# Performance work log

Measured on AMD Instinct MI355X. Metric: run time of the kernel, lower is better.

Reference implementation:

```python
import jax, jax.numpy as jnp
import numpy as np
import math

B, S, D, H, DH = 1, 2048, 2048, 16, 64  # batch, seq, d_model, n_heads, d_head
LAMBDA_INIT = 0.8
EPS = 1e-5


def setup_inputs() -> dict:
    key = jax.random.key(0)
    ks = jax.random.split(key, 10)
    w_scale = 0.02
    inner = 2 * DH * H  # == D here
    return {
        "x": jax.random.normal(ks[0], (B, S, D), dtype=jnp.float32),
        "Wq": jax.random.normal(ks[1], (D, inner), dtype=jnp.float32) * w_scale,
        "Wk": jax.random.normal(ks[2], (D, inner), dtype=jnp.float32) * w_scale,
        "Wv": jax.random.normal(ks[3], (D, inner), dtype=jnp.float32) * w_scale,
        "Wo": jax.random.normal(ks[4], (inner, D), dtype=jnp.float32) * w_scale,
        "lambda_q1": jax.random.normal(ks[5], (DH,), dtype=jnp.float32) * 0.1,
        "lambda_k1": jax.random.normal(ks[6], (DH,), dtype=jnp.float32) * 0.1,
        "lambda_q2": jax.random.normal(ks[7], (DH,), dtype=jnp.float32) * 0.1,
        "lambda_k2": jax.random.normal(ks[8], (DH,), dtype=jnp.float32) * 0.1,
        "gn_weight": jnp.ones((inner,), dtype=jnp.float32),
        "gn_bias": jnp.zeros((inner,), dtype=jnp.float32),
    }


def reference(x, Wq, Wk, Wv, Wo, lambda_q1, lambda_k1, lambda_q2, lambda_k2,
              gn_weight, gn_bias):
    b, s, _ = x.shape
    dh = lambda_q1.shape[0]
    h = Wq.shape[1] // (2 * dh)
    scale = 1.0 / math.sqrt(dh)

    q = (x @ Wq).reshape(b, s, h, 2, dh)
    k = (x @ Wk).reshape(b, s, h, 2, dh)
    v = (x @ Wv).reshape(b, s, h, 2 * dh)

    # [B,H,S,dh]
    q1 = jnp.swapaxes(q[..., 0, :], 1, 2)
    q2 = jnp.swapaxes(q[..., 1, :], 1, 2)
    k1 = jnp.swapaxes(k[..., 0, :], 1, 2)
    k2 = jnp.swapaxes(k[..., 1, :], 1, 2)
    vh = jnp.swapaxes(v, 1, 2)  # [B,H,S,2*dh]

    score1 = jnp.einsum("bhsd,bhtd->bhst", q1, k1) * scale
    score2 = jnp.einsum("bhsd,bhtd->bhst", q2, k2) * scale
    attn1 = jax.nn.softmax(score1, axis=-1)
    attn2 = jax.nn.softmax(score2, axis=-1)

    lam = (jnp.exp(jnp.sum(lambda_q1 * lambda_k1))
           - jnp.exp(jnp.sum(lambda_q2 * lambda_k2)) + LAMBDA_INIT)

    out = jnp.einsum("bhst,bhtd->bhsd", attn1 - lam * attn2, vh)  # [B,H,S,2dh]
    out = jnp.swapaxes(out, 1, 2)  # [B,S,H,2dh]

    # GroupNorm: n_heads groups over the channel dim, per token
    mu = jnp.mean(out, axis=-1, keepdims=True)
    var = jnp.var(out, axis=-1, keepdims=True)
    out = (out - mu) * jax.lax.rsqrt(var + EPS)
    gw = gn_weight.reshape(h, 2 * dh)
    gb = gn_bias.reshape(h, 2 * dh)
    out = out * gw + gb

    out = out * (1.0 - LAMBDA_INIT)
    return out.reshape(b, s, -1) @ Wo
```

## Files before the change

### kernel.cpp

```cpp
#include <hip/hip_runtime.h>
#include <hip/hip_bf16.h>

typedef unsigned short u16;
typedef __attribute__((ext_vector_type(8))) short short8;
typedef __attribute__((ext_vector_type(4))) short short4v;
typedef __attribute__((ext_vector_type(4))) float f32x4;

#define S_DIM 2048
#define D_DIM 2048
#define H_NUM 16
#define DH_NUM 64

#if __has_builtin(__builtin_amdgcn_exp2f)
#define EXP2(x) __builtin_amdgcn_exp2f(x)
#else
#define EXP2(x) exp2f(x)
#endif

__device__ __forceinline__ u16 f2bf(float f) {
    union { float f; unsigned u; } x; x.f = f;
    unsigned r = x.u + 0x7fff + ((x.u >> 16) & 1);
    return (u16)(r >> 16);
}

__device__ __forceinline__ unsigned pk_bf16(float a, float b) {
    union { __hip_bfloat162 h; unsigned u; } cv;
    float2 t; t.x = a; t.y = b;
    cv.h = __float22bfloat162_rn(t);
    return cv.u;
}

__device__ __forceinline__ void lane_swap32(unsigned &a, unsigned &b) {
    asm("v_permlane32_swap_b32 %0, %1" : "+v"(a), "+v"(b));
}
__device__ __forceinline__ void lane_swap16(unsigned &a, unsigned &b) {
    asm("v_permlane16_swap_b32 %0, %1" : "+v"(a), "+v"(b));
}

__device__ __forceinline__ void gload16(const void* g, void* l) {
    __builtin_amdgcn_global_load_lds(
        (const __attribute__((address_space(1))) unsigned int*)g,
        (__attribute__((address_space(3))) unsigned int*)l, 16, 0, 0);
}

__device__ __forceinline__ void transpose_body(const float* __restrict__ src,
                                               u16* __restrict__ dst,
                                               int tx, int ty, int t)
{
    __shared__ float tile[64][65];
    const int r0 = ty * 64, c0 = tx * 64;
#pragma unroll
    for (int p = 0; p < 4; ++p) {
        int r = p * 16 + (t >> 4), c = (t & 15) * 4;
        float4 v = *(const float4*)&src[(long)(r0 + r) * D_DIM + c0 + c];
        tile[r][c] = v.x; tile[r][c + 1] = v.y;
        tile[r][c + 2] = v.z; tile[r][c + 3] = v.w;
    }
    __syncthreads();
#pragma unroll
    for (int p = 0; p < 2; ++p) {
        int ch = t + p * 256;
        int i = ch >> 3, j0 = (ch & 7) * 8;
        short8 o;
#pragma unroll
        for (int jj = 0; jj < 8; ++jj)
            o[jj] = (short)f2bf(tile[j0 + jj][i]);
        *(short8*)&dst[(long)(c0 + i) * D_DIM + r0 + j0] = o;
    }
}

__global__ __launch_bounds__(256)
void transpose_fast(const float* __restrict__ src, u16* __restrict__ dst)
{
    transpose_body(src, dst, blockIdx.x, blockIdx.y, threadIdx.x);
}

__global__ __launch_bounds__(256)
void prep4(const float* __restrict__ x,
           const float* __restrict__ Wq, const float* __restrict__ Wk,
           const float* __restrict__ Wv,
           u16* __restrict__ XB, u16* T0, u16* T1, u16* T2)
{
    const int z = blockIdx.z, t = threadIdx.x, bx = blockIdx.x;
    if (z == 0) {
        long i0 = ((long)bx * 256 + t) * 16;
        short8 o0, o1;
#pragma unroll
        for (int j = 0; j < 2; ++j) {
            float4 a = *(const float4*)&x[i0 + j * 8];
            float4 b = *(const float4*)&x[i0 + j * 8 + 4];
            short8& o = j ? o1 : o0;
            o[0] = (short)f2bf(a.x); o[1] = (short)f2bf(a.y);
            o[2] = (short)f2bf(a.z); o[3] = (short)f2bf(a.w);
            o[4] = (short)f2bf(b.x); o[5] = (short)f2bf(b.y);
            o[6] = (short)f2bf(b.z); o[7] = (short)f2bf(b.w);
        }
        *(short8*)&XB[i0] = o0;
        *(short8*)&XB[i0 + 8] = o1;
    } else {
        const float* src = (z == 1) ? Wq : (z == 2) ? Wk : Wv;
        u16* dst         = (z == 1) ? T0 : (z == 2) ? T1 : T2;
        transpose_body(src, dst, bx & 31, bx >> 5, t);
    }
}

__global__ __launch_bounds__(256)
void cvt_bf16(const float* __restrict__ src, u16* __restrict__ dst)
{
    int i = (blockIdx.x * 256 + threadIdx.x) * 4;
    float4 v = *(const float4*)(src + i);
    ushort4 o;
    o.x = f2bf(v.x); o.y = f2bf(v.y); o.z = f2bf(v.z); o.w = f2bf(v.w);
    *(ushort4*)(dst + i) = o;
}

__global__ __launch_bounds__(256, 2)
void gemm128(const u16* __restrict__ A,
             const u16* B0, const u16* B1, const u16* B2,
             u16* C0, u16* C1, u16* C2, int zbase)
{
    const int Kd = D_DIM, N = D_DIM, M = S_DIM;
    const int z = blockIdx.z + zbase;
    const u16* Bt = (z == 0) ? B0 : (z == 1) ? B1 : B2;
    u16* C        = (z == 0) ? C0 : (z == 1) ? C1 : C2;

    __shared__ __attribute__((aligned(16))) u16 As[128 * 64];
    __shared__ __attribute__((aligned(16))) u16 Bs[128 * 64];

    const int tid = threadIdx.x, lane = tid & 63, wave = tid >> 6;
    const int bm = blockIdx.x * 128, bn = blockIdx.y * 128;

    const int grow = lane >> 3;
    const int gcol = ((lane & 7) ^ grow) * 8;

    const int wr = (wave >> 1) * 64, wc = (wave & 1) * 64;
    const int fr = lane & 15, fq = lane >> 4;
    const int swz = fr & 7;

    f32x4 acc[4][4];
    for (int i = 0; i < 4; ++i)
        for (int j = 0; j < 4; ++j) { f32x4 zz = {0.f,0.f,0.f,0.f}; acc[i][j] = zz; }

    for (int k0 = 0; k0 < Kd; k0 += 64) {
#pragma unroll
        for (int g = 0; g < 4; ++g) {
            int r = wave * 32 + g * 8;
            gload16(A + (long)(bm + r + grow) * Kd + k0 + gcol, &As[r * 64]);
            gload16(Bt + (long)(bn + r + grow) * Kd + k0 + gcol, &Bs[r * 64]);
        }
        __syncthreads();

#pragma unroll
        for (int ks = 0; ks < 2; ++ks) {
            const int slot = ((fq + ks * 4) ^ swz) * 8;
            short8 af[4], bf[4];
#pragma unroll
            for (int i = 0; i < 4; ++i) {
                af[i] = *(const short8*)&As[(wr + i * 16 + fr) * 64 + slot];
                bf[i] = *(const short8*)&Bs[(wc + i * 16 + fr) * 64 + slot];
            }
            if (z == 2) {
#pragma unroll
                for (int i = 0; i < 4; ++i)
#pragma unroll
                    for (int j = 0; j < 4; ++j)
                        acc[i][j] = __builtin_amdgcn_mfma_f32_16x16x32_bf16(bf[j], af[i], acc[i][j], 0, 0, 0);
            } else {
#pragma unroll
                for (int i = 0; i < 4; ++i)
#pragma unroll
                    for (int j = 0; j < 4; ++j)
                        acc[i][j] = __builtin_amdgcn_mfma_f32_16x16x32_bf16(af[i], bf[j], acc[i][j], 0, 0, 0);
            }
        }
        __syncthreads();
    }

    if (z == 2) {
#pragma unroll
        for (int i = 0; i < 4; ++i) {
            int tok = bm + wr + i * 16 + fr;
#pragma unroll
            for (int j = 0; j < 4; ++j) {
                int ch = bn + wc + j * 16 + fq * 4;
#pragma unroll
                for (int r = 0; r < 4; ++r)
                    C[(long)(ch + r) * M + tok] = f2bf(acc[i][j][r]);
            }
        }
    } else {
        const float sc = (z == 0) ? 0.125f * 1.44269504f : 1.0f;
#pragma unroll
        for (int i = 0; i < 4; ++i) {
            int row = bm + wr + i * 16 + fq * 4;
#pragma unroll
            for (int j = 0; j < 4; ++j) {
                int col = bn + wc + j * 16 + fr;
#pragma unroll
                for (int r = 0; r < 4; ++r)
                    C[(long)(row + r) * N + col] = f2bf(acc[i][j][r] * sc);
            }
        }
    }
}

__global__ __launch_bounds__(256, 2)
void gemm_out(const u16* __restrict__ A, const u16* __restrict__ Bt,
              float* __restrict__ C)
{
    const int Kd = D_DIM, N = D_DIM;

    __shared__ __attribute__((aligned(16))) u16 As[64 * 64];
    __shared__ __attribute__((aligned(16))) u16 Bs[128 * 64];

    const int tid = threadIdx.x, lane = tid & 63, wave = tid >> 6;
    const int bm = blockIdx.x * 64, bn = blockIdx.y * 128;

    const int grow = lane >> 3;
    const int gcol = ((lane & 7) ^ grow) * 8;

    const int wr = (wave >> 1) * 32, wc = (wave & 1) * 64;
    const int fr = lane & 15, fq = lane >> 4;
    const int swz = fr & 7;

    f32x4 acc[2][4];
    for (int i = 0; i < 2; ++i)
        for (int j = 0; j < 4; ++j) { f32x4 zz = {0.f,0.f,0.f,0.f}; acc[i][j] = zz; }

    for (int k0 = 0; k0 < Kd; k0 += 64) {
#pragma unroll
        for (int g = 0; g < 2; ++g) {
            int r = wave * 16 + g * 8;
            gload16(A + (long)(bm + r + grow) * Kd + k0 + gcol, &As[r * 64]);
        }
#pragma unroll
        for (int g = 0; g < 4; ++g) {
            int r = wave * 32 + g * 8;
            gload16(Bt + (long)(bn + r + grow) * Kd + k0 + gcol, &Bs[r * 64]);
        }
        __syncthreads();

#pragma unroll
        for (int ks = 0; ks < 2; ++ks) {
            const int slot = ((fq + ks * 4) ^ swz) * 8;
            short8 af[2], bf[4];
#pragma unroll
            for (int i = 0; i < 2; ++i)
                af[i] = *(const short8*)&As[(wr + i * 16 + fr) * 64 + slot];
#pragma unroll
            for (int j = 0; j < 4; ++j)
                bf[j] = *(const short8*)&Bs[(wc + j * 16 + fr) * 64 + slot];
#pragma unroll
            for (int i = 0; i < 2; ++i)
#pragma unroll
                for (int j = 0; j < 4; ++j)
                    acc[i][j] = __builtin_amdgcn_mfma_f32_16x16x32_bf16(af[i], bf[j], acc[i][j], 0, 0, 0);
        }
        __syncthreads();
    }

#pragma unroll
    for (int i = 0; i < 2; ++i) {
        int row = bm + wr + i * 16 + fq * 4;
#pragma unroll
        for (int j = 0; j < 4; ++j) {
            int col = bn + wc + j * 16 + fr;
#pragma unroll
            for (int r = 0; r < 4; ++r)
                C[(long)(row + r) * N + col] = acc[i][j][r];
        }
    }
}

__global__ __launch_bounds__(256, 2)
void diff_attn(const u16* __restrict__ Qm, const u16* __restrict__ Km,
               const u16* __restrict__ Vt,
               const float* __restrict__ lq1, const float* __restrict__ lk1,
               const float* __restrict__ lq2, const float* __restrict__ lk2,
               const float* __restrict__ gw, const float* __restrict__ gb,
               u16* __restrict__ Y)
{
    __shared__ __attribute__((aligned(16))) u16 K1s[2][64 * 64];
    __shared__ __attribute__((aligned(16))) u16 K2s[2][64 * 64];
    __shared__ __attribute__((aligned(16))) u16 Vts[2][128 * 64];

    const int tid = threadIdx.x, lane = tid & 63, wave = tid >> 6;
    const int h = blockIdx.y;
    const int q0 = blockIdx.x * 64 + wave * 16;
    const int fr = lane & 15, qq = lane >> 4;
    const int fsw = fr & 7;

    const int grow = lane >> 3;
    const int gcol = ((lane & 7) ^ grow) * 8;

    float d1 = 0.f, d2 = 0.f;
    for (int i = 0; i < DH_NUM; ++i) {
        d1 += lq1[i] * lk1[i];
        d2 += lq2[i] * lk2[i];
    }
    const float lam = __expf(d1) - __expf(d2) + 0.8f;

    short8 q1f[2], q2f[2];
    {
        const u16* qb = Qm + (long)(q0 + fr) * D_DIM + h * 128;
        q1f[0] = *(const short8*)(qb + qq * 8);
        q1f[1] = *(const short8*)(qb + 32 + qq * 8);
        q2f[0] = *(const short8*)(qb + 64 + qq * 8);
        q2f[1] = *(const short8*)(qb + 96 + qq * 8);
    }

    f32x4 a1[8], a2[8];
    for (int n = 0; n < 8; ++n) { f32x4 zz = {0.f,0.f,0.f,0.f}; a1[n] = zz; a2[n] = zz; }
    float ls1 = 0.f, ls2 = 0.f;

    auto stage = [&](int kb, int b) {
        const long kbase = (long)(kb * 64) * D_DIM + h * 128;
#pragma unroll
        for (int g = 0; g < 2; ++g) {
            int r = wave * 16 + g * 8;
            gload16(Km + kbase + (long)(r + grow) * D_DIM + gcol,      &K1s[b][r * 64]);
            gload16(Km + kbase + (long)(r + grow) * D_DIM + 64 + gcol, &K2s[b][r * 64]);
        }
#pragma unroll
        for (int g = 0; g < 4; ++g) {
            int c = wave * 32 + g * 8;
            gload16(Vt + (long)(h * 128 + c + grow) * S_DIM + kb * 64 + gcol,
                    &Vts[b][c * 64]);
        }
    };

    stage(0, 0);
    int p = 0;

    for (int kb = 0; kb < S_DIM / 64; ++kb) {
        __syncthreads();
        const bool more = (kb + 1 < S_DIM / 64);
        if (more) stage(kb + 1, p ^ 1);

#pragma unroll
        for (int jj = 0; jj < 2; ++jj) {
            unsigned u1[2][2], u2[2][2];
#pragma unroll
            for (int jh = 0; jh < 2; ++jh) {
                const int j = jj * 2 + jh;
                f32x4 s1 = {0.f,0.f,0.f,0.f}, s2 = {0.f,0.f,0.f,0.f};
#pragma unroll
                for (int ks = 0; ks < 2; ++ks) {
                    const int slot = ((ks * 4 + qq) ^ fsw) * 8;
                    short8 k1 = *(const short8*)&K1s[p][(j * 16 + fr) * 64 + slot];
                    short8 k2 = *(const short8*)&K2s[p][(j * 16 + fr) * 64 + slot];
                    s1 = __builtin_amdgcn_mfma_f32_16x16x32_bf16(k1, q1f[ks], s1, 0, 0, 0);
                    s2 = __builtin_amdgcn_mfma_f32_16x16x32_bf16(k2, q2f[ks], s2, 0, 0, 0);
                }
                float e1[4], e2[4];
#pragma unroll
                for (int r = 0; r < 4; ++r) {
                    e1[r] = EXP2(s1[r]);
                    e2[r] = EXP2(s2[r]);
                    ls1 += e1[r]; ls2 += e2[r];
                }
                u1[jh][0] = pk_bf16(e1[0], e1[1]); u1[jh][1] = pk_bf16(e1[2], e1[3]);
                u2[jh][0] = pk_bf16(e2[0], e2[1]); u2[jh][1] = pk_bf16(e2[2], e2[3]);
            }

            union { short8 s; unsigned u[4]; } F1, F2;
            {
                unsigned x = u1[0][0], y = u1[1][0];
                lane_swap32(x, y); lane_swap16(x, y);
                F1.u[0] = x; F1.u[2] = y;
            }
            {
                unsigned x = u1[0][1], y = u1[1][1];
                lane_swap32(x, y); lane_swap16(x, y);
                F1.u[1] = x; F1.u[3] = y;
            }
            {
                unsigned x = u2[0][0], y = u2[1][0];
                lane_swap32(x, y); lane_swap16(x, y);
                F2.u[0] = x; F2.u[2] = y;
            }
            {
                unsigned x = u2[0][1], y = u2[1][1];
                lane_swap32(x, y); lane_swap16(x, y);
                F2.u[1] = x; F2.u[3] = y;
            }

            const int slotV = ((jj * 4 + qq) ^ fsw) * 8;
            __builtin_amdgcn_s_setprio(1);
#pragma unroll
            for (int n = 0; n < 8; ++n) {
                short8 vf = *(const short8*)&Vts[p][(n * 16 + fr) * 64 + slotV];
                a1[n] = __builtin_amdgcn_mfma_f32_16x16x32_bf16(vf, F1.s, a1[n], 0, 0, 0);
                a2[n] = __builtin_amdgcn_mfma_f32_16x16x32_bf16(vf, F2.s, a2[n], 0, 0, 0);
            }
            __builtin_amdgcn_s_setprio(0);
        }

        p ^= 1;
    }

    float L1 = ls1, L2 = ls2;
    L1 += __shfl_xor(L1, 16, 64); L1 += __shfl_xor(L1, 32, 64);
    L2 += __shfl_xor(L2, 16, 64); L2 += __shfl_xor(L2, 32, 64);
    const float i1 = 1.f / L1, i2 = lam / L2;

    float o[8][4], sum = 0.f, sq = 0.f;
#pragma unroll
    for (int n = 0; n < 8; ++n)
#pragma unroll
        for (int r = 0; r < 4; ++r) {
            float v = a1[n][r] * i1 - a2[n][r] * i2;
            o[n][r] = v; sum += v; sq += v * v;
        }
    sum += __shfl_xor(sum, 16, 64); sum += __shfl_xor(sum, 32, 64);
    sq  += __shfl_xor(sq, 16, 64);  sq  += __shfl_xor(sq, 32, 64);
    const float mean = sum * (1.f / 128.f);
    const float var = sq * (1.f / 128.f) - mean * mean;
    const float inv = rsqrtf(var + 1e-5f);

    const long yrow = (long)(q0 + fr) * D_DIM + h * 128;
#pragma unroll
    for (int n = 0; n < 8; ++n) {
        float4 g4 = *(const float4*)&gw[h * 128 + n * 16 + qq * 4];
        float4 b4 = *(const float4*)&gb[h * 128 + n * 16 + qq * 4];
        ushort4 st;
        st.x = f2bf(((o[n][0] - mean) * inv * g4.x + b4.x) * 0.2f);
        st.y = f2bf(((o[n][1] - mean) * inv * g4.y + b4.y) * 0.2f);
        st.z = f2bf(((o[n][2] - mean) * inv * g4.z + b4.z) * 0.2f);
        st.w = f2bf(((o[n][3] - mean) * inv * g4.w + b4.w) * 0.2f);
        *(ushort4*)&Y[yrow + n * 16 + qq * 4] = st;
    }
}

extern "C" void kernel_launch(void* const* d_in, const int* in_sizes, int n_in,
                              void* d_out, int out_size, void* d_ws, size_t ws_size,
                              hipStream_t stream)
{
    const float* x   = (const float*)d_in[0];
    const float* Wq  = (const float*)d_in[1];
    const float* Wk  = (const float*)d_in[2];
    const float* Wv  = (const float*)d_in[3];
    const float* Wo  = (const float*)d_in[4];
    const float* lq1 = (const float*)d_in[5];
    const float* lk1 = (const float*)d_in[6];
    const float* lq2 = (const float*)d_in[7];
    const float* lk2 = (const float*)d_in[8];
    const float* gw  = (const float*)d_in[9];
    const float* gb  = (const float*)d_in[10];

    char* ws = (char*)d_ws;
    const size_t SEG = (size_t)D_DIM * D_DIM * sizeof(u16);
    const dim3 tgrid(32, 32), agrid(32, 16), ogrid(32, 16);

    if (ws_size >= 7 * SEG) {
        u16* XB  = (u16*)(ws + 0 * SEG);
        u16* WTq = (u16*)(ws + 1 * SEG);
        u16* WTk = (u16*)(ws + 2 * SEG);
        u16* WTv = (u16*)(ws + 3 * SEG);
        u16* Qb  = (u16*)(ws + 4 * SEG);
        u16* Kb  = (u16*)(ws + 5 * SEG);
        u16* Vt  = (u16*)(ws + 6 * SEG);
        u16* WTo = WTq;
        u16* Yb  = WTk;

        prep4<<<dim3(1024, 1, 4), 256, 0, stream>>>(x, Wq, Wk, Wv,
                                                    XB, WTq, WTk, WTv);
        gemm128<<<dim3(16, 16, 3), 256, 0, stream>>>(XB, WTq, WTk, WTv,
                                                     Qb, Kb, Vt, 0);
        transpose_fast<<<tgrid, 256, 0, stream>>>(Wo, WTo);
        diff_attn<<<agrid, 256, 0, stream>>>(Qb, Kb, Vt, lq1, lk1, lq2, lk2,
                                             gw, gb, Yb);
        gemm_out<<<ogrid, 256, 0, stream>>>(Yb, WTo, (float*)d_out);
    } else {
        u16* XB = (u16*)(ws + 0 * SEG);
        u16* WT = (u16*)(ws + 1 * SEG);
        u16* Qb = (u16*)(ws + 2 * SEG);
        u16* Kb = (u16*)(ws + 3 * SEG);
        u16* Vt = (u16*)(ws + 4 * SEG);

        cvt_bf16<<<4096, 256, 0, stream>>>(x, XB);
        transpose_fast<<<tgrid, 256, 0, stream>>>(Wq, WT);
        gemm128<<<dim3(16, 16, 1), 256, 0, stream>>>(XB, WT, WT, WT, Qb, Qb, Qb, 0);
        transpose_fast<<<tgrid, 256, 0, stream>>>(Wk, WT);
        gemm128<<<dim3(16, 16, 1), 256, 0, stream>>>(XB, WT, WT, WT, Kb, Kb, Kb, 1);
        transpose_fast<<<tgrid, 256, 0, stream>>>(Wv, WT);
        gemm128<<<dim3(16, 16, 1), 256, 0, stream>>>(XB, WT, WT, WT, Vt, Vt, Vt, 2);
        diff_attn<<<agrid, 256, 0, stream>>>(Qb, Kb, Vt, lq1, lk1, lq2, lk2,
                                             gw, gb, XB);
        transpose_fast<<<tgrid, 256, 0, stream>>>(Wo, WT);
        gemm_out<<<ogrid, 256, 0, stream>>>(XB, WT, (float*)d_out);
    }
}
```

Measured before the change: 299.8 us.

## Split attention key blocks across two wave groups and fold Wo transpose into prep

The attention kernel now runs 512 threads per block. Two groups of four waves each take half of every 64-key block, and their partial PV accumulators and row sums are combined through shared memory before the GroupNorm epilogue. This doubles the waves available to hide latency and the exp/MFMA dependency chains per query tile, at the cost of an extra reduction pass, more shared memory traffic and half the threads idling in the epilogue. Separately, when the workspace allows eight segments, the Wo transpose is folded into the prep kernel as a fifth z-slice, which removes one launch.

```diff
diff --git a/kernel.cpp b/kernel.cpp
--- a/kernel.cpp
+++ b/kernel.cpp
@@ -78,8 +78,8 @@
 __global__ __launch_bounds__(256)
 void prep4(const float* __restrict__ x,
            const float* __restrict__ Wq, const float* __restrict__ Wk,
-           const float* __restrict__ Wv,
-           u16* __restrict__ XB, u16* T0, u16* T1, u16* T2)
+           const float* __restrict__ Wv, const float* __restrict__ Wo,
+           u16* __restrict__ XB, u16* T0, u16* T1, u16* T2, u16* T3)
 {
     const int z = blockIdx.z, t = threadIdx.x, bx = blockIdx.x;
     if (z == 0) {
@@ -98,8 +98,8 @@
         *(short8*)&XB[i0] = o0;
         *(short8*)&XB[i0 + 8] = o1;
     } else {
-        const float* src = (z == 1) ? Wq : (z == 2) ? Wk : Wv;
-        u16* dst         = (z == 1) ? T0 : (z == 2) ? T1 : T2;
+        const float* src = (z == 1) ? Wq : (z == 2) ? Wk : (z == 3) ? Wv : Wo;
+        u16* dst         = (z == 1) ? T0 : (z == 2) ? T1 : (z == 3) ? T2 : T3;
         transpose_body(src, dst, bx & 31, bx >> 5, t);
     }
 }
@@ -272,7 +272,7 @@
     }
 }
 
-__global__ __launch_bounds__(256, 2)
+__global__ __launch_bounds__(512, 4)
 void diff_attn(const u16* __restrict__ Qm, const u16* __restrict__ Km,
                const u16* __restrict__ Vt,
                const float* __restrict__ lq1, const float* __restrict__ lk1,
@@ -280,13 +280,14 @@
                const float* __restrict__ gw, const float* __restrict__ gb,
                u16* __restrict__ Y)
 {
-    __shared__ __attribute__((aligned(16))) u16 K1s[2][64 * 64];
-    __shared__ __attribute__((aligned(16))) u16 K2s[2][64 * 64];
-    __shared__ __attribute__((aligned(16))) u16 Vts[2][128 * 64];
+    __shared__ __attribute__((aligned(16))) u16 SM[2][16384];
+    __shared__ float lsb[2][4][64];
 
     const int tid = threadIdx.x, lane = tid & 63, wave = tid >> 6;
+    const int sub = wave >> 2;
+    const int wq  = wave & 3;
     const int h = blockIdx.y;
-    const int q0 = blockIdx.x * 64 + wave * 16;
+    const int q0 = blockIdx.x * 64 + wq * 16;
     const int fr = lane & 15, qq = lane >> 4;
     const int fsw = fr & 7;
 
@@ -315,86 +316,81 @@
 
     auto stage = [&](int kb, int b) {
         const long kbase = (long)(kb * 64) * D_DIM + h * 128;
+        const int r = wave * 8;
+        gload16(Km + kbase + (long)(r + grow) * D_DIM + gcol,      &SM[b][r * 64]);
+        gload16(Km + kbase + (long)(r + grow) * D_DIM + 64 + gcol, &SM[b][4096 + r * 64]);
 #pragma unroll
         for (int g = 0; g < 2; ++g) {
-            int r = wave * 16 + g * 8;
-            gload16(Km + kbase + (long)(r + grow) * D_DIM + gcol,      &K1s[b][r * 64]);
-            gload16(Km + kbase + (long)(r + grow) * D_DIM + 64 + gcol, &K2s[b][r * 64]);
-        }
-#pragma unroll
-        for (int g = 0; g < 4; ++g) {
-            int c = wave * 32 + g * 8;
+            int c = wave * 16 + g * 8;
             gload16(Vt + (long)(h * 128 + c + grow) * S_DIM + kb * 64 + gcol,
-                    &Vts[b][c * 64]);
+                    &SM[b][8192 + c * 64]);
         }
     };
 
     stage(0, 0);
     int p = 0;
 
+    const int jj = sub;
     for (int kb = 0; kb < S_DIM / 64; ++kb) {
         __syncthreads();
         const bool more = (kb + 1 < S_DIM / 64);
         if (more) stage(kb + 1, p ^ 1);
 
-#pragma unroll
-        for (int jj = 0; jj < 2; ++jj) {
-            unsigned u1[2][2], u2[2][2];
-#pragma unroll
-            for (int jh = 0; jh < 2; ++jh) {
-                const int j = jj * 2 + jh;
-                f32x4 s1 = {0.f,0.f,0.f,0.f}, s2 = {0.f,0.f,0.f,0.f};
-#pragma unroll
-                for (int ks = 0; ks < 2; ++ks) {
-                    const int slot = ((ks * 4 + qq) ^ fsw) * 8;
-                    short8 k1 = *(const short8*)&K1s[p][(j * 16 + fr) * 64 + slot];
-                    short8 k2 = *(const short8*)&K2s[p][(j * 16 + fr) * 64 + slot];
-                    s1 = __builtin_amdgcn_mfma_f32_16x16x32_bf16(k1, q1f[ks], s1, 0, 0, 0);
-                    s2 = __builtin_amdgcn_mfma_f32_16x16x32_bf16(k2, q2f[ks], s2, 0, 0, 0);
-                }
-                float e1[4], e2[4];
-#pragma unroll
-                for (int r = 0; r < 4; ++r) {
-                    e1[r] = EXP2(s1[r]);
-                    e2[r] = EXP2(s2[r]);
-                    ls1 += e1[r]; ls2 += e2[r];
-                }
-                u1[jh][0] = pk_bf16(e1[0], e1[1]); u1[jh][1] = pk_bf16(e1[2], e1[3]);
-                u2[jh][0] = pk_bf16(e2[0], e2[1]); u2[jh][1] = pk_bf16(e2[2], e2[3]);
+        unsigned u1[2][2], u2[2][2];
+#pragma unroll
+        for (int jh = 0; jh < 2; ++jh) {
+            const int j = jj * 2 + jh;
+            f32x4 s1 = {0.f,0.f,0.f,0.f}, s2 = {0.f,0.f,0.f,0.f};
+#pragma unroll
+            for (int ks = 0; ks < 2; ++ks) {
+                const int slot = ((ks * 4 + qq) ^ fsw) * 8;
+                short8 k1 = *(const short8*)&SM[p][(j * 16 + fr) * 64 + slot];
+                short8 k2 = *(const short8*)&SM[p][4096 + (j * 16 + fr) * 64 + slot];
+                s1 = __builtin_amdgcn_mfma_f32_16x16x32_bf16(k1, q1f[ks], s1, 0, 0, 0);
+                s2 = __builtin_amdgcn_mfma_f32_16x16x32_bf16(k2, q2f[ks], s2, 0, 0, 0);
             }
-
-            union { short8 s; unsigned u[4]; } F1, F2;
-            {
-                unsigned x = u1[0][0], y = u1[1][0];
-                lane_swap32(x, y); lane_swap16(x, y);
-                F1.u[0] = x; F1.u[2] = y;
+            float e1[4], e2[4];
+#pragma unroll
+            for (int r = 0; r < 4; ++r) {
+                e1[r] = EXP2(s1[r]);
+                e2[r] = EXP2(s2[r]);
+                ls1 += e1[r]; ls2 += e2[r];
             }
-            {
-                unsigned x = u1[0][1], y = u1[1][1];
-                lane_swap32(x, y); lane_swap16(x, y);
-                F1.u[1] = x; F1.u[3] = y;
-            }
-            {
-                unsigned x = u2[0][0], y = u2[1][0];
-                lane_swap32(x, y); lane_swap16(x, y);
-                F2.u[0] = x; F2.u[2] = y;
-            }
-            {
-                unsigned x = u2[0][1], y = u2[1][1];
-                lane_swap32(x, y); lane_swap16(x, y);
-                F2.u[1] = x; F2.u[3] = y;
-            }
-
-            const int slotV = ((jj * 4 + qq) ^ fsw) * 8;
-            __builtin_amdgcn_s_setprio(1);
-#pragma unroll
-            for (int n = 0; n < 8; ++n) {
-                short8 vf = *(const short8*)&Vts[p][(n * 16 + fr) * 64 + slotV];
-                a1[n] = __builtin_amdgcn_mfma_f32_16x16x32_bf16(vf, F1.s, a1[n], 0, 0, 0);
-                a2[n] = __builtin_amdgcn_mfma_f32_16x16x32_bf16(vf, F2.s, a2[n], 0, 0, 0);
-            }
-            __builtin_amdgcn_s_setprio(0);
-        }
+            u1[jh][0] = pk_bf16(e1[0], e1[1]); u1[jh][1] = pk_bf16(e1[2], e1[3]);
+            u2[jh][0] = pk_bf16(e2[0], e2[1]); u2[jh][1] = pk_bf16(e2[2], e2[3]);
+        }
+
+        union { short8 s; unsigned u[4]; } F1, F2;
+        {
+            unsigned x = u1[0][0], y = u1[1][0];
+            lane_swap32(x, y); lane_swap16(x, y);
+            F1.u[0] = x; F1.u[2] = y;
+        }
+        {
+            unsigned x = u1[0][1], y = u1[1][1];
+            lane_swap32(x, y); lane_swap16(x, y);
+            F1.u[1] = x; F1.u[3] = y;
+        }
+        {
+            unsigned x = u2[0][0], y = u2[1][0];
+            lane_swap32(x, y); lane_swap16(x, y);
+            F2.u[0] = x; F2.u[2] = y;
+        }
+        {
+            unsigned x = u2[0][1], y = u2[1][1];
+            lane_swap32(x, y); lane_swap16(x, y);
+            F2.u[1] = x; F2.u[3] = y;
+        }
+
+        const int slotV = ((jj * 4 + qq) ^ fsw) * 8;
+        __builtin_amdgcn_s_setprio(1);
+#pragma unroll
+        for (int n = 0; n < 8; ++n) {
+            short8 vf = *(const short8*)&SM[p][8192 + (n * 16 + fr) * 64 + slotV];
+            a1[n] = __builtin_amdgcn_mfma_f32_16x16x32_bf16(vf, F1.s, a1[n], 0, 0, 0);
+            a2[n] = __builtin_amdgcn_mfma_f32_16x16x32_bf16(vf, F2.s, a2[n], 0, 0, 0);
+        }
+        __builtin_amdgcn_s_setprio(0);
 
         p ^= 1;
     }
@@ -402,6 +398,29 @@
     float L1 = ls1, L2 = ls2;
     L1 += __shfl_xor(L1, 16, 64); L1 += __shfl_xor(L1, 32, 64);
     L2 += __shfl_xor(L2, 16, 64); L2 += __shfl_xor(L2, 32, 64);
+
+    __syncthreads();
+    float* cb = (float*)&SM[0][0];
+    const int cbase = (wq * 64 + lane) * 64;
+    if (sub == 1) {
+#pragma unroll
+        for (int n = 0; n < 8; ++n) {
+            *(f32x4*)&cb[cbase + n * 4]      = a1[n];
+            *(f32x4*)&cb[cbase + 32 + n * 4] = a2[n];
+        }
+        lsb[0][wq][lane] = L1;
+        lsb[1][wq][lane] = L2;
+    }
+    __syncthreads();
+    if (sub == 1) return;
+
+#pragma unroll
+    for (int n = 0; n < 8; ++n) {
+        a1[n] += *(const f32x4*)&cb[cbase + n * 4];
+        a2[n] += *(const f32x4*)&cb[cbase + 32 + n * 4];
+    }
+    L1 += lsb[0][wq][lane];
+    L2 += lsb[1][wq][lane];
     const float i1 = 1.f / L1, i2 = lam / L2;
 
     float o[8][4], sum = 0.f, sq = 0.f;
@@ -452,7 +471,25 @@
     const size_t SEG = (size_t)D_DIM * D_DIM * sizeof(u16);
     const dim3 tgrid(32, 32), agrid(32, 16), ogrid(32, 16);
 
-    if (ws_size >= 7 * SEG) {
+    if (ws_size >= 8 * SEG) {
+        u16* XB  = (u16*)(ws + 0 * SEG);
+        u16* WTq = (u16*)(ws + 1 * SEG);
+        u16* WTk = (u16*)(ws + 2 * SEG);
+        u16* WTv = (u16*)(ws + 3 * SEG);
+        u16* Qb  = (u16*)(ws + 4 * SEG);
+        u16* Kb  = (u16*)(ws + 5 * SEG);
+        u16* Vt  = (u16*)(ws + 6 * SEG);
+        u16* WTo = (u16*)(ws + 7 * SEG);
+        u16* Yb  = WTk;
+
+        prep4<<<dim3(1024, 1, 5), 256, 0, stream>>>(x, Wq, Wk, Wv, Wo,
+                                                    XB, WTq, WTk, WTv, WTo);
+        gemm128<<<dim3(16, 16, 3), 256, 0, stream>>>(XB, WTq, WTk, WTv,
+                                                     Qb, Kb, Vt, 0);
+        diff_attn<<<agrid, 512, 0, stream>>>(Qb, Kb, Vt, lq1, lk1, lq2, lk2,
+                                             gw, gb, Yb);
+        gemm_out<<<ogrid, 256, 0, stream>>>(Yb, WTo, (float*)d_out);
+    } else if (ws_size >= 7 * SEG) {
         u16* XB  = (u16*)(ws + 0 * SEG);
         u16* WTq = (u16*)(ws + 1 * SEG);
         u16* WTk = (u16*)(ws + 2 * SEG);
@@ -463,12 +500,12 @@
         u16* WTo = WTq;
         u16* Yb  = WTk;
 
-        prep4<<<dim3(1024, 1, 4), 256, 0, stream>>>(x, Wq, Wk, Wv,
-                                                    XB, WTq, WTk, WTv);
+        prep4<<<dim3(1024, 1, 4), 256, 0, stream>>>(x, Wq, Wk, Wv, Wo,
+                                                    XB, WTq, WTk, WTv, WTq);
         gemm128<<<dim3(16, 16, 3), 256, 0, stream>>>(XB, WTq, WTk, WTv,
                                                      Qb, Kb, Vt, 0);
         transpose_fast<<<tgrid, 256, 0, stream>>>(Wo, WTo);
-        diff_attn<<<agrid, 256, 0, stream>>>(Qb, Kb, Vt, lq1, lk1, lq2, lk2,
+        diff_attn<<<agrid, 512, 0, stream>>>(Qb, Kb, Vt, lq1, lk1, lq2, lk2,
                                              gw, gb, Yb);
         gemm_out<<<ogrid, 256, 0, stream>>>(Yb, WTo, (float*)d_out);
     } else {
@@ -485,7 +522,7 @@
         gemm128<<<dim3(16, 16, 1), 256, 0, stream>>>(XB, WT, WT, WT, Kb, Kb, Kb, 1);
         transpose_fast<<<tgrid, 256, 0, stream>>>(Wv, WT);
         gemm128<<<dim3(16, 16, 1), 256, 0, stream>>>(XB, WT, WT, WT, Vt, Vt, Vt, 2);
-        diff_attn<<<agrid, 256, 0, stream>>>(Qb, Kb, Vt, lq1, lk1, lq2, lk2,
+        diff_attn<<<agrid, 512, 0, stream>>>(Qb, Kb, Vt, lq1, lk1, lq2, lk2,
                                              gw, gb, XB);
         transpose_fast<<<tgrid, 256, 0, stream>>>(Wo, WT);
         gemm_out<<<ogrid, 256, 0, stream>>>(XB, WT, (float*)d_out);
```

Result: no change. 303.9 us (+1.4%).

## Double-buffer LDS in GEMMs and fold Wo transpose into prep kernel

Applied to the files above, without the earlier changes.

Both GEMM kernels now keep two LDS buffers, load the next K tile while computing on the current one, and need one barrier per iteration instead of two. When the workspace is large enough, the Wo transpose joins the fused prep launch as a fifth z slice with its own buffer, which removes one kernel launch. Double buffering doubles shared memory per block (gemm128 goes to 64KB), which may lower occupancy under the two-blocks-per-SM launch bound.

```diff
diff --git a/kernel.cpp b/kernel.cpp
--- a/kernel.cpp
+++ b/kernel.cpp
@@ -78,8 +78,8 @@
 __global__ __launch_bounds__(256)
 void prep4(const float* __restrict__ x,
            const float* __restrict__ Wq, const float* __restrict__ Wk,
-           const float* __restrict__ Wv,
-           u16* __restrict__ XB, u16* T0, u16* T1, u16* T2)
+           const float* __restrict__ Wv, const float* __restrict__ Wo,
+           u16* __restrict__ XB, u16* T0, u16* T1, u16* T2, u16* T3)
 {
     const int z = blockIdx.z, t = threadIdx.x, bx = blockIdx.x;
     if (z == 0) {
@@ -98,8 +98,8 @@
         *(short8*)&XB[i0] = o0;
         *(short8*)&XB[i0 + 8] = o1;
     } else {
-        const float* src = (z == 1) ? Wq : (z == 2) ? Wk : Wv;
-        u16* dst         = (z == 1) ? T0 : (z == 2) ? T1 : T2;
+        const float* src = (z == 1) ? Wq : (z == 2) ? Wk : (z == 3) ? Wv : Wo;
+        u16* dst         = (z == 1) ? T0 : (z == 2) ? T1 : (z == 3) ? T2 : T3;
         transpose_body(src, dst, bx & 31, bx >> 5, t);
     }
 }
@@ -124,8 +124,8 @@
     const u16* Bt = (z == 0) ? B0 : (z == 1) ? B1 : B2;
     u16* C        = (z == 0) ? C0 : (z == 1) ? C1 : C2;
 
-    __shared__ __attribute__((aligned(16))) u16 As[128 * 64];
-    __shared__ __attribute__((aligned(16))) u16 Bs[128 * 64];
+    __shared__ __attribute__((aligned(16))) u16 As[2][128 * 64];
+    __shared__ __attribute__((aligned(16))) u16 Bs[2][128 * 64];
 
     const int tid = threadIdx.x, lane = tid & 63, wave = tid >> 6;
     const int bm = blockIdx.x * 128, bn = blockIdx.y * 128;
@@ -141,14 +141,22 @@
     for (int i = 0; i < 4; ++i)
         for (int j = 0; j < 4; ++j) { f32x4 zz = {0.f,0.f,0.f,0.f}; acc[i][j] = zz; }
 
-    for (int k0 = 0; k0 < Kd; k0 += 64) {
+    auto stage = [&](int k0, int b) {
 #pragma unroll
         for (int g = 0; g < 4; ++g) {
             int r = wave * 32 + g * 8;
-            gload16(A + (long)(bm + r + grow) * Kd + k0 + gcol, &As[r * 64]);
-            gload16(Bt + (long)(bn + r + grow) * Kd + k0 + gcol, &Bs[r * 64]);
-        }
+            gload16(A + (long)(bm + r + grow) * Kd + k0 + gcol, &As[b][r * 64]);
+            gload16(Bt + (long)(bn + r + grow) * Kd + k0 + gcol, &Bs[b][r * 64]);
+        }
+    };
+
+    stage(0, 0);
+    int p = 0;
+    const int NT = Kd / 64;
+
+    for (int t = 0; t < NT; ++t) {
         __syncthreads();
+        if (t + 1 < NT) stage((t + 1) * 64, p ^ 1);
 
 #pragma unroll
         for (int ks = 0; ks < 2; ++ks) {
@@ -156,8 +164,8 @@
             short8 af[4], bf[4];
 #pragma unroll
             for (int i = 0; i < 4; ++i) {
-                af[i] = *(const short8*)&As[(wr + i * 16 + fr) * 64 + slot];
-                bf[i] = *(const short8*)&Bs[(wc + i * 16 + fr) * 64 + slot];
+                af[i] = *(const short8*)&As[p][(wr + i * 16 + fr) * 64 + slot];
+                bf[i] = *(const short8*)&Bs[p][(wc + i * 16 + fr) * 64 + slot];
             }
             if (z == 2) {
 #pragma unroll
@@ -173,7 +181,7 @@
                         acc[i][j] = __builtin_amdgcn_mfma_f32_16x16x32_bf16(af[i], bf[j], acc[i][j], 0, 0, 0);
             }
         }
-        __syncthreads();
+        p ^= 1;
     }
 
     if (z == 2) {
@@ -210,8 +218,8 @@
 {
     const int Kd = D_DIM, N = D_DIM;
 
-    __shared__ __attribute__((aligned(16))) u16 As[64 * 64];
-    __shared__ __attribute__((aligned(16))) u16 Bs[128 * 64];
+    __shared__ __attribute__((aligned(16))) u16 As[2][64 * 64];
+    __shared__ __attribute__((aligned(16))) u16 Bs[2][128 * 64];
 
     const int tid = threadIdx.x, lane = tid & 63, wave = tid >> 6;
     const int bm = blockIdx.x * 64, bn = blockIdx.y * 128;
@@ -227,18 +235,26 @@
     for (int i = 0; i < 2; ++i)
         for (int j = 0; j < 4; ++j) { f32x4 zz = {0.f,0.f,0.f,0.f}; acc[i][j] = zz; }
 
-    for (int k0 = 0; k0 < Kd; k0 += 64) {
+    auto stage = [&](int k0, int b) {
 #pragma unroll
         for (int g = 0; g < 2; ++g) {
             int r = wave * 16 + g * 8;
-            gload16(A + (long)(bm + r + grow) * Kd + k0 + gcol, &As[r * 64]);
+            gload16(A + (long)(bm + r + grow) * Kd + k0 + gcol, &As[b][r * 64]);
         }
 #pragma unroll
         for (int g = 0; g < 4; ++g) {
             int r = wave * 32 + g * 8;
-            gload16(Bt + (long)(bn + r + grow) * Kd + k0 + gcol, &Bs[r * 64]);
-        }
+            gload16(Bt + (long)(bn + r + grow) * Kd + k0 + gcol, &Bs[b][r * 64]);
+        }
+    };
+
+    stage(0, 0);
+    int p = 0;
+    const int NT = Kd / 64;
+
+    for (int t = 0; t < NT; ++t) {
         __syncthreads();
+        if (t + 1 < NT) stage((t + 1) * 64, p ^ 1);
 
 #pragma unroll
         for (int ks = 0; ks < 2; ++ks) {
@@ -246,17 +262,17 @@
             short8 af[2], bf[4];
 #pragma unroll
             for (int i = 0; i < 2; ++i)
-                af[i] = *(const short8*)&As[(wr + i * 16 + fr) * 64 + slot];
+                af[i] = *(const short8*)&As[p][(wr + i * 16 + fr) * 64 + slot];
 #pragma unroll
             for (int j = 0; j < 4; ++j)
-                bf[j] = *(const short8*)&Bs[(wc + j * 16 + fr) * 64 + slot];
+                bf[j] = *(const short8*)&Bs[p][(wc + j * 16 + fr) * 64 + slot];
 #pragma unroll
             for (int i = 0; i < 2; ++i)
 #pragma unroll
                 for (int j = 0; j < 4; ++j)
                     acc[i][j] = __builtin_amdgcn_mfma_f32_16x16x32_bf16(af[i], bf[j], acc[i][j], 0, 0, 0);
         }
-        __syncthreads();
+        p ^= 1;
     }
 
 #pragma unroll
@@ -452,7 +468,25 @@
     const size_t SEG = (size_t)D_DIM * D_DIM * sizeof(u16);
     const dim3 tgrid(32, 32), agrid(32, 16), ogrid(32, 16);
 
-    if (ws_size >= 7 * SEG) {
+    if (ws_size >= 8 * SEG) {
+        u16* XB  = (u16*)(ws + 0 * SEG);
+        u16* WTq = (u16*)(ws + 1 * SEG);
+        u16* WTk = (u16*)(ws + 2 * SEG);
+        u16* WTv = (u16*)(ws + 3 * SEG);
+        u16* Qb  = (u16*)(ws + 4 * SEG);
+        u16* Kb  = (u16*)(ws + 5 * SEG);
+        u16* Vt  = (u16*)(ws + 6 * SEG);
+        u16* WTo = (u16*)(ws + 7 * SEG);
+        u16* Yb  = WTk;
+
+        prep4<<<dim3(1024, 1, 5), 256, 0, stream>>>(x, Wq, Wk, Wv, Wo,
+                                                    XB, WTq, WTk, WTv, WTo);
+        gemm128<<<dim3(16, 16, 3), 256, 0, stream>>>(XB, WTq, WTk, WTv,
+                                                     Qb, Kb, Vt, 0);
+        diff_attn<<<agrid, 256, 0, stream>>>(Qb, Kb, Vt, lq1, lk1, lq2, lk2,
+                                             gw, gb, Yb);
+        gemm_out<<<ogrid, 256, 0, stream>>>(Yb, WTo, (float*)d_out);
+    } else if (ws_size >= 7 * SEG) {
         u16* XB  = (u16*)(ws + 0 * SEG);
         u16* WTq = (u16*)(ws + 1 * SEG);
         u16* WTk = (u16*)(ws + 2 * SEG);
@@ -463,8 +497,8 @@
         u16* WTo = WTq;
         u16* Yb  = WTk;
 
-        prep4<<<dim3(1024, 1, 4), 256, 0, stream>>>(x, Wq, Wk, Wv,
-                                                    XB, WTq, WTk, WTv);
+        prep4<<<dim3(1024, 1, 4), 256, 0, stream>>>(x, Wq, Wk, Wv, Wo,
+                                                    XB, WTq, WTk, WTv, WTq);
         gemm128<<<dim3(16, 16, 3), 256, 0, stream>>>(XB, WTq, WTk, WTv,
                                                      Qb, Kb, Vt, 0);
         transpose_fast<<<tgrid, 256, 0, stream>>>(Wo, WTo);
```

New measurement: 296.8 us. No clear change (-1.0%).

## Fold Wo transpose into prep kernel and shrink output GEMM tiles

Applied to the files above, without the earlier changes.

When the workspace holds an eighth segment, the Wo transpose moves into the batched prep4 launch, which saves one kernel launch. The output GEMM tile drops from 64x128 to 64x64, doubling the grid to 1024 blocks, with a higher launch-bounds occupancy hint. gemm128 also gets a higher occupancy hint, which may force register spills. The smaller output tiles fill the GPU better but reload the A operand more often.

```diff
diff --git a/kernel.cpp b/kernel.cpp
--- a/kernel.cpp
+++ b/kernel.cpp
@@ -78,8 +78,8 @@
 __global__ __launch_bounds__(256)
 void prep4(const float* __restrict__ x,
            const float* __restrict__ Wq, const float* __restrict__ Wk,
-           const float* __restrict__ Wv,
-           u16* __restrict__ XB, u16* T0, u16* T1, u16* T2)
+           const float* __restrict__ Wv, const float* __restrict__ Wo,
+           u16* __restrict__ XB, u16* T0, u16* T1, u16* T2, u16* T3)
 {
     const int z = blockIdx.z, t = threadIdx.x, bx = blockIdx.x;
     if (z == 0) {
@@ -98,8 +98,8 @@
         *(short8*)&XB[i0] = o0;
         *(short8*)&XB[i0 + 8] = o1;
     } else {
-        const float* src = (z == 1) ? Wq : (z == 2) ? Wk : Wv;
-        u16* dst         = (z == 1) ? T0 : (z == 2) ? T1 : T2;
+        const float* src = (z == 1) ? Wq : (z == 2) ? Wk : (z == 3) ? Wv : Wo;
+        u16* dst         = (z == 1) ? T0 : (z == 2) ? T1 : (z == 3) ? T2 : T3;
         transpose_body(src, dst, bx & 31, bx >> 5, t);
     }
 }
@@ -114,7 +114,7 @@
     *(ushort4*)(dst + i) = o;
 }
 
-__global__ __launch_bounds__(256, 2)
+__global__ __launch_bounds__(256, 3)
 void gemm128(const u16* __restrict__ A,
              const u16* B0, const u16* B1, const u16* B2,
              u16* C0, u16* C1, u16* C2, int zbase)
@@ -204,38 +204,34 @@
     }
 }
 
-__global__ __launch_bounds__(256, 2)
+__global__ __launch_bounds__(256, 4)
 void gemm_out(const u16* __restrict__ A, const u16* __restrict__ Bt,
               float* __restrict__ C)
 {
     const int Kd = D_DIM, N = D_DIM;
 
     __shared__ __attribute__((aligned(16))) u16 As[64 * 64];
-    __shared__ __attribute__((aligned(16))) u16 Bs[128 * 64];
+    __shared__ __attribute__((aligned(16))) u16 Bs[64 * 64];
 
     const int tid = threadIdx.x, lane = tid & 63, wave = tid >> 6;
-    const int bm = blockIdx.x * 64, bn = blockIdx.y * 128;
+    const int bm = blockIdx.x * 64, bn = blockIdx.y * 64;
 
     const int grow = lane >> 3;
     const int gcol = ((lane & 7) ^ grow) * 8;
 
-    const int wr = (wave >> 1) * 32, wc = (wave & 1) * 64;
+    const int wr = (wave >> 1) * 32, wc = (wave & 1) * 32;
     const int fr = lane & 15, fq = lane >> 4;
     const int swz = fr & 7;
 
-    f32x4 acc[2][4];
+    f32x4 acc[2][2];
     for (int i = 0; i < 2; ++i)
-        for (int j = 0; j < 4; ++j) { f32x4 zz = {0.f,0.f,0.f,0.f}; acc[i][j] = zz; }
+        for (int j = 0; j < 2; ++j) { f32x4 zz = {0.f,0.f,0.f,0.f}; acc[i][j] = zz; }
 
     for (int k0 = 0; k0 < Kd; k0 += 64) {
 #pragma unroll
         for (int g = 0; g < 2; ++g) {
             int r = wave * 16 + g * 8;
             gload16(A + (long)(bm + r + grow) * Kd + k0 + gcol, &As[r * 64]);
-        }
-#pragma unroll
-        for (int g = 0; g < 4; ++g) {
-            int r = wave * 32 + g * 8;
             gload16(Bt + (long)(bn + r + grow) * Kd + k0 + gcol, &Bs[r * 64]);
         }
         __syncthreads();
@@ -243,17 +239,16 @@
 #pragma unroll
         for (int ks = 0; ks < 2; ++ks) {
             const int slot = ((fq + ks * 4) ^ swz) * 8;
-            short8 af[2], bf[4];
+            short8 af[2], bf[2];
+#pragma unroll
+            for (int i = 0; i < 2; ++i) {
+                af[i] = *(const short8*)&As[(wr + i * 16 + fr) * 64 + slot];
+                bf[i] = *(const short8*)&Bs[(wc + i * 16 + fr) * 64 + slot];
+            }
 #pragma unroll
             for (int i = 0; i < 2; ++i)
-                af[i] = *(const short8*)&As[(wr + i * 16 + fr) * 64 + slot];
-#pragma unroll
-            for (int j = 0; j < 4; ++j)
-                bf[j] = *(const short8*)&Bs[(wc + j * 16 + fr) * 64 + slot];
-#pragma unroll
-            for (int i = 0; i < 2; ++i)
-#pragma unroll
-                for (int j = 0; j < 4; ++j)
+#pragma unroll
+                for (int j = 0; j < 2; ++j)
                     acc[i][j] = __builtin_amdgcn_mfma_f32_16x16x32_bf16(af[i], bf[j], acc[i][j], 0, 0, 0);
         }
         __syncthreads();
@@ -263,7 +258,7 @@
     for (int i = 0; i < 2; ++i) {
         int row = bm + wr + i * 16 + fq * 4;
 #pragma unroll
-        for (int j = 0; j < 4; ++j) {
+        for (int j = 0; j < 2; ++j) {
             int col = bn + wc + j * 16 + fr;
 #pragma unroll
             for (int r = 0; r < 4; ++r)
@@ -450,9 +445,27 @@
 
     char* ws = (char*)d_ws;
     const size_t SEG = (size_t)D_DIM * D_DIM * sizeof(u16);
-    const dim3 tgrid(32, 32), agrid(32, 16), ogrid(32, 16);
-
-    if (ws_size >= 7 * SEG) {
+    const dim3 tgrid(32, 32), agrid(32, 16), ogrid(32, 32);
+
+    if (ws_size >= 8 * SEG) {
+        u16* XB  = (u16*)(ws + 0 * SEG);
+        u16* WTq = (u16*)(ws + 1 * SEG);
+        u16* WTk = (u16*)(ws + 2 * SEG);
+        u16* WTv = (u16*)(ws + 3 * SEG);
+        u16* Qb  = (u16*)(ws + 4 * SEG);
+        u16* Kb  = (u16*)(ws + 5 * SEG);
+        u16* Vt  = (u16*)(ws + 6 * SEG);
+        u16* WTo = (u16*)(ws + 7 * SEG);
+        u16* Yb  = WTk;
+
+        prep4<<<dim3(1024, 1, 5), 256, 0, stream>>>(x, Wq, Wk, Wv, Wo,
+                                                    XB, WTq, WTk, WTv, WTo);
+        gemm128<<<dim3(16, 16, 3), 256, 0, stream>>>(XB, WTq, WTk, WTv,
+                                                     Qb, Kb, Vt, 0);
+        diff_attn<<<agrid, 256, 0, stream>>>(Qb, Kb, Vt, lq1, lk1, lq2, lk2,
+                                             gw, gb, Yb);
+        gemm_out<<<ogrid, 256, 0, stream>>>(Yb, WTo, (float*)d_out);
+    } else if (ws_size >= 7 * SEG) {
         u16* XB  = (u16*)(ws + 0 * SEG);
         u16* WTq = (u16*)(ws + 1 * SEG);
         u16* WTk = (u16*)(ws + 2 * SEG);
@@ -463,8 +476,8 @@
         u16* WTo = WTq;
         u16* Yb  = WTk;
 
-        prep4<<<dim3(1024, 1, 4), 256, 0, stream>>>(x, Wq, Wk, Wv,
-                                                    XB, WTq, WTk, WTv);
+        prep4<<<dim3(1024, 1, 4), 256, 0, stream>>>(x, Wq, Wk, Wv, Wo,
+                                                    XB, WTq, WTk, WTv, WTq);
         gemm128<<<dim3(16, 16, 3), 256, 0, stream>>>(XB, WTq, WTk, WTv,
                                                      Qb, Kb, Vt, 0);
         transpose_fast<<<tgrid, 256, 0, stream>>>(Wo, WTo);
```

After: 364.9 us. 21.7% more time.
